# Kernel optimization log

Measured on AMD Instinct MI355X. Metric: run time of the kernel, lower is better.

## Reference

```python
import jax, jax.numpy as jnp
import numpy as np

B, A, D, K = 262144, 10, 10, 32  # batch, aspects, aspect dim (=10), projection dim


def setup_inputs() -> dict:
    key = jax.random.key(0)
    ks = jax.random.split(key, 7)
    scale = 0.01
    return {
        "user_rep": jax.random.normal(ks[0], (B, A, D), jnp.float32),
        "item_rep": jax.random.normal(ks[1], (B, A, D), jnp.float32),
        "affinity_matrix": jax.random.uniform(ks[2], (D, D), jnp.float32, -scale, scale),
        "user_projection": jax.random.uniform(ks[3], (K, D), jnp.float32, -scale, scale),
        "user_parameters": jax.random.uniform(ks[4], (K, 1), jnp.float32, -scale, scale),
        "item_projection": jax.random.uniform(ks[5], (K, D), jnp.float32, -scale, scale),
        "item_parameters": jax.random.uniform(ks[6], (K, 1), jnp.float32, -scale, scale),
    }


def reference(user_rep, item_rep, affinity_matrix, user_projection,
              user_parameters, item_projection, item_parameters):
    # affinity: relu( U @ M @ V^T )  -> [B, Au, Av]
    aff = jax.nn.relu(jnp.einsum('bud,de,bve->buv', user_rep, affinity_matrix, item_rep))

    h_user = jnp.einsum('kd,bud->bku', user_projection, user_rep)  # [B,K,Au]
    h_item = jnp.einsum('kd,bvd->bkv', item_projection, item_rep)  # [B,K,Av]

    # user importance branch
    hu = jax.nn.relu(h_user + jnp.einsum('bkv,buv->bku', h_item, aff))
    u_score = jnp.einsum('k,bku->bu', user_parameters[:, 0], hu)   # [B,Au]
    user_asp_importance = jax.nn.softmax(u_score, axis=1)

    # item importance branch
    hi = jax.nn.relu(h_item + jnp.einsum('bku,buv->bkv', h_user, aff))
    i_score = jnp.einsum('k,bkv->bv', item_parameters[:, 0], hi)   # [B,Av]
    item_asp_importance = jax.nn.softmax(i_score, axis=1)

    return (user_asp_importance, item_asp_importance)
```

## Files before the change

kernel.cpp:

```cpp
#include <hip/hip_runtime.h>
#include <hip/hip_bf16.h>

#define NB 262144
#define AA 10
#define DD 10
#define KK 32

static __device__ __forceinline__ float b2f(unsigned short h) {
    union { unsigned u; float f; } c; c.u = ((unsigned)h) << 16; return c.f;
}
static __device__ __forceinline__ float bflo(unsigned w) {
    union { unsigned u; float f; } c; c.u = w << 16; return c.f;
}
static __device__ __forceinline__ float bfhi(unsigned w) {
    union { unsigned u; float f; } c; c.u = w & 0xffff0000u; return c.f;
}

__device__ __forceinline__ int detect_f32(const unsigned short* p, int nshorts,
                                          unsigned expthr, int lane) {
    int bad = 0;
    if (lane < nshorts) {
        unsigned e = (p[lane] >> 7) & 0xFFu;
        bad = (e >= expthr);
    }
    return __any(bad);
}

__global__ __launch_bounds__(64, 1) void aie_kernel(
    const unsigned short* __restrict__ user_rep,
    const unsigned short* __restrict__ item_rep,
    const unsigned short* __restrict__ wM,
    const unsigned short* __restrict__ wPu,
    const unsigned short* __restrict__ wpu,
    const unsigned short* __restrict__ wPi,
    const unsigned short* __restrict__ wpi,
    float* __restrict__ out)
{
    __shared__ float sM[100];
    __shared__ float sPu[KK * DD], sPi[KK * DD], spu[KK], spi[KK];
    __shared__ float buf[6400];

    const int t = threadIdx.x;

    int f = 0;
    f |= detect_f32(user_rep, 64, 137, t) << 0;
    f |= detect_f32(item_rep, 64, 137, t) << 1;
    f |= detect_f32(wM,  64, 125, t) << 2;
    f |= detect_f32(wPu, 64, 125, t) << 3;
    f |= detect_f32(wpu, 32, 125, t) << 4;
    f |= detect_f32(wPi, 64, 125, t) << 5;
    f |= detect_f32(wpi, 32, 125, t) << 6;

    {
        const float* fM  = (const float*)wM;
        const float* fPu = (const float*)wPu;
        const float* fPi = (const float*)wPi;
        const float* fpu = (const float*)wpu;
        const float* fpi = (const float*)wpi;
        for (int i = t; i < 100; i += 64) sM[i] = (f & 4) ? fM[i] : b2f(wM[i]);
        for (int i = t; i < KK * DD; i += 64) {
            sPu[i] = (f & 8)  ? fPu[i] : b2f(wPu[i]);
            sPi[i] = (f & 32) ? fPi[i] : b2f(wPi[i]);
        }
        if (t < KK) {
            spu[t] = (f & 16) ? fpu[t] : b2f(wpu[t]);
            spi[t] = (f & 64) ? fpi[t] : b2f(wpi[t]);
        }
    }
    __syncthreads();

    const int blk = blockIdx.x;
    float U[AA][DD], V[AA][DD];

    if (f & 2) {
        const float4* g = (const float4*)((const float*)item_rep + (size_t)blk * 6400);
        #pragma unroll
        for (int j = 0; j < 25; j++) ((float4*)buf)[t + 64 * j] = g[t + 64 * j];
    } else {
        const uint2* g = (const uint2*)(item_rep + (size_t)blk * 6400);
        #pragma unroll
        for (int j = 0; j < 25; j++) {
            uint2 w = g[t + 64 * j];
            ((float4*)buf)[t + 64 * j] =
                make_float4(bflo(w.x), bfhi(w.x), bflo(w.y), bfhi(w.y));
        }
    }
    __syncthreads();
    {
        const float4* mine = (const float4*)(buf + 100 * t);
        #pragma unroll
        for (int j = 0; j < 25; j++) {
            float4 w = mine[j]; int e = 4 * j;
            V[e / 10][e % 10]             = w.x;
            V[(e + 1) / 10][(e + 1) % 10] = w.y;
            V[(e + 2) / 10][(e + 2) % 10] = w.z;
            V[(e + 3) / 10][(e + 3) % 10] = w.w;
        }
    }
    __syncthreads();

    if (f & 1) {
        const float4* g = (const float4*)((const float*)user_rep + (size_t)blk * 6400);
        #pragma unroll
        for (int j = 0; j < 25; j++) ((float4*)buf)[t + 64 * j] = g[t + 64 * j];
    } else {
        const uint2* g = (const uint2*)(user_rep + (size_t)blk * 6400);
        #pragma unroll
        for (int j = 0; j < 25; j++) {
            uint2 w = g[t + 64 * j];
            ((float4*)buf)[t + 64 * j] =
                make_float4(bflo(w.x), bfhi(w.x), bflo(w.y), bfhi(w.y));
        }
    }
    __syncthreads();
    {
        const float4* mine = (const float4*)(buf + 100 * t);
        #pragma unroll
        for (int j = 0; j < 25; j++) {
            float4 w = mine[j]; int e = 4 * j;
            U[e / 10][e % 10]             = w.x;
            U[(e + 1) / 10][(e + 1) % 10] = w.y;
            U[(e + 2) / 10][(e + 2) % 10] = w.z;
            U[(e + 3) / 10][(e + 3) % 10] = w.w;
        }
    }
    __syncthreads();

    float W[AA][DD];
    #pragma unroll
    for (int u = 0; u < AA; u++) {
        float um[DD];
        #pragma unroll
        for (int e = 0; e < DD; e++) {
            float a = U[u][0] * sM[e];
            #pragma unroll
            for (int d = 1; d < DD; d++) a += U[u][d] * sM[d * 10 + e];
            um[e] = a;
        }
        float wrow[DD];
        #pragma unroll
        for (int d = 0; d < DD; d++) wrow[d] = 0.f;
        #pragma unroll
        for (int v = 0; v < AA; v++) {
            float r = um[0] * V[v][0];
            #pragma unroll
            for (int e = 1; e < DD; e++) r += um[e] * V[v][e];
            r = fmaxf(r, 0.f);
            #pragma unroll
            for (int d = 0; d < DD; d++) wrow[d] += r * V[v][d];
        }
        #pragma unroll
        for (int d = 0; d < DD; d++) W[u][d] = wrow[d];
    }

    float us[AA];
    #pragma unroll
    for (int u = 0; u < AA; u++) us[u] = 0.f;
    #pragma unroll 2
    for (int k = 0; k < KK; k++) {
        float pu[DD], pi[DD];
        #pragma unroll
        for (int d = 0; d < DD; d++) { pu[d] = sPu[k * 10 + d]; pi[d] = sPi[k * 10 + d]; }
        const float wk = spu[k];
        #pragma unroll
        for (int u = 0; u < AA; u++) {
            float a = pu[0] * U[u][0], b = pi[0] * W[u][0];
            #pragma unroll
            for (int d = 1; d < DD; d++) { a += pu[d] * U[u][d]; b += pi[d] * W[u][d]; }
            us[u] += wk * fmaxf(a + b, 0.f);
        }
    }

    {
        float mx = us[0];
        #pragma unroll
        for (int u = 1; u < AA; u++) mx = fmaxf(mx, us[u]);
        float s = 0.f;
        #pragma unroll
        for (int u = 0; u < AA; u++) { us[u] = __expf(us[u] - mx); s += us[u]; }
        float inv = 1.f / s;
        #pragma unroll
        for (int u = 0; u < AA; u++) buf[11 * t + u] = us[u] * inv;
    }

    float X[AA][DD];
    #pragma unroll
    for (int u = 0; u < AA; u++) {
        float um[DD];
        #pragma unroll
        for (int e = 0; e < DD; e++) {
            float a = U[u][DD - 1] * sM[(DD - 1) * 10 + e];
            #pragma unroll
            for (int d = DD - 2; d >= 0; d--) a += U[u][d] * sM[d * 10 + e];
            um[e] = a;
        }
        #pragma unroll
        for (int v = 0; v < AA; v++) {
            float r = um[DD - 1] * V[v][DD - 1];
            #pragma unroll
            for (int e = DD - 2; e >= 0; e--) r += um[e] * V[v][e];
            r = fmaxf(r, 0.f);
            #pragma unroll
            for (int d = 0; d < DD; d++) {
                if (u == 0) X[v][d] = r * U[u][d];
                else        X[v][d] += r * U[u][d];
            }
        }
    }

    float isc[AA];
    #pragma unroll
    for (int v = 0; v < AA; v++) isc[v] = 0.f;
    #pragma unroll 2
    for (int k = 0; k < KK; k++) {
        float pu[DD], pi[DD];
        #pragma unroll
        for (int d = 0; d < DD; d++) { pu[d] = sPu[k * 10 + d]; pi[d] = sPi[k * 10 + d]; }
        const float wk = spi[k];
        #pragma unroll
        for (int v = 0; v < AA; v++) {
            float a = pi[0] * V[v][0], b = pu[0] * X[v][0];
            #pragma unroll
            for (int d = 1; d < DD; d++) { a += pi[d] * V[v][d]; b += pu[d] * X[v][d]; }
            isc[v] += wk * fmaxf(a + b, 0.f);
        }
    }

    {
        float mx = isc[0];
        #pragma unroll
        for (int v = 1; v < AA; v++) mx = fmaxf(mx, isc[v]);
        float s = 0.f;
        #pragma unroll
        for (int v = 0; v < AA; v++) { isc[v] = __expf(isc[v] - mx); s += isc[v]; }
        float inv = 1.f / s;
        #pragma unroll
        for (int v = 0; v < AA; v++) buf[704 + 11 * t + v] = isc[v] * inv;
    }
    __syncthreads();

    {
        float2* o0 = (float2*)(out + (size_t)blk * 640);
        float2* o1 = (float2*)(out + (size_t)NB * 10 + (size_t)blk * 640);
        #pragma unroll
        for (int j = 0; j < 5; j++) {
            int m = t + 64 * j;
            int i = m / 5;
            int u = 2 * (m - 5 * i);
            o0[m] = make_float2(buf[11 * i + u],       buf[11 * i + u + 1]);
            o1[m] = make_float2(buf[704 + 11 * i + u], buf[704 + 11 * i + u + 1]);
        }
    }
}

extern "C" void kernel_launch(void* const* d_in, const int* in_sizes, int n_in,
                              void* d_out, int out_size, void* d_ws, size_t ws_size,
                              hipStream_t stream) {
    const unsigned short* user_rep = (const unsigned short*)d_in[0];
    const unsigned short* item_rep = (const unsigned short*)d_in[1];
    const unsigned short* wM       = (const unsigned short*)d_in[2];
    const unsigned short* wPu      = (const unsigned short*)d_in[3];
    const unsigned short* wpu      = (const unsigned short*)d_in[4];
    const unsigned short* wPi      = (const unsigned short*)d_in[5];
    const unsigned short* wpi      = (const unsigned short*)d_in[6];
    float* out                     = (float*)d_out;

    dim3 block(64);
    dim3 grid(NB / 64);
    hipLaunchKernelGGL(aie_kernel, grid, block, 0, stream,
                       user_rep, item_rep, wM, wPu, wpu, wPi, wpi, out);
}
```

Before: 393.2 us.

## Split weight prep kernel, use packed float2 math, fuse K loop into per-aspect rows

Moves weight dtype detection and conversion into a separate one-block kernel that writes fp32 weights to workspace, which the main kernel reads as uniform global loads instead of staging them in shared memory. The main kernel loads each row's inputs directly per thread, with no shared-memory transpose or block barriers, and stores them as float2 vectors so the math can use packed FP32 ops. The K-projection loop is fused per aspect so the W/X intermediates no longer need full 10x10 register arrays, which lowers register pressure and lets launch bounds allow two waves. The costs are uncoalesced strided global loads per thread and an extra kernel launch.

```diff
diff --git a/kernel.cpp b/kernel.cpp
--- a/kernel.cpp
+++ b/kernel.cpp
@@ -1,11 +1,12 @@
 #include <hip/hip_runtime.h>
-#include <hip/hip_bf16.h>
 
 #define NB 262144
 #define AA 10
 #define DD 10
 #define KK 32
 
+typedef float v2f __attribute__((ext_vector_type(2)));
+
 static __device__ __forceinline__ float b2f(unsigned short h) {
     union { unsigned u; float f; } c; c.u = ((unsigned)h) << 16; return c.f;
 }
@@ -14,6 +15,9 @@
 }
 static __device__ __forceinline__ float bfhi(unsigned w) {
     union { unsigned u; float f; } c; c.u = w & 0xffff0000u; return c.f;
+}
+static __device__ __forceinline__ v2f mk2(float a, float b) {
+    v2f r; r.x = a; r.y = b; return r;
 }
 
 __device__ __forceinline__ int detect_f32(const unsigned short* p, int nshorts,
@@ -26,229 +30,213 @@
     return __any(bad);
 }
 
-__global__ __launch_bounds__(64, 1) void aie_kernel(
-    const unsigned short* __restrict__ user_rep,
-    const unsigned short* __restrict__ item_rep,
+__global__ __launch_bounds__(64) void prep_weights(
     const unsigned short* __restrict__ wM,
     const unsigned short* __restrict__ wPu,
     const unsigned short* __restrict__ wpu,
     const unsigned short* __restrict__ wPi,
     const unsigned short* __restrict__ wpi,
+    float* __restrict__ wf)
+{
+    const int t = threadIdx.x;
+    int f = 0;
+    f |= detect_f32(wM,  64, 125, t) << 0;
+    f |= detect_f32(wPu, 64, 125, t) << 1;
+    f |= detect_f32(wpu, 32, 125, t) << 2;
+    f |= detect_f32(wPi, 64, 125, t) << 3;
+    f |= detect_f32(wpi, 32, 125, t) << 4;
+    const float* fM  = (const float*)wM;
+    const float* fPu = (const float*)wPu;
+    const float* fpu = (const float*)wpu;
+    const float* fPi = (const float*)wPi;
+    const float* fpi = (const float*)wpi;
+    for (int i = t; i < 100; i += 64) wf[i]       = (f & 1)  ? fM[i]  : b2f(wM[i]);
+    for (int i = t; i < 320; i += 64) wf[100 + i] = (f & 2)  ? fPu[i] : b2f(wPu[i]);
+    if (t < 32)                       wf[420 + t] = (f & 4)  ? fpu[t] : b2f(wpu[t]);
+    for (int i = t; i < 320; i += 64) wf[452 + i] = (f & 8)  ? fPi[i] : b2f(wPi[i]);
+    if (t < 32)                       wf[772 + t] = (f & 16) ? fpi[t] : b2f(wpi[t]);
+}
+
+__global__ __launch_bounds__(64, 2) void aie_main(
+    const unsigned short* __restrict__ user_rep,
+    const unsigned short* __restrict__ item_rep,
+    const float* __restrict__ wf,
     float* __restrict__ out)
 {
-    __shared__ float sM[100];
-    __shared__ float sPu[KK * DD], sPi[KK * DD], spu[KK], spi[KK];
-    __shared__ float buf[6400];
-
+    __shared__ float obuf[1408];
     const int t = threadIdx.x;
-
-    int f = 0;
-    f |= detect_f32(user_rep, 64, 137, t) << 0;
-    f |= detect_f32(item_rep, 64, 137, t) << 1;
-    f |= detect_f32(wM,  64, 125, t) << 2;
-    f |= detect_f32(wPu, 64, 125, t) << 3;
-    f |= detect_f32(wpu, 32, 125, t) << 4;
-    f |= detect_f32(wPi, 64, 125, t) << 5;
-    f |= detect_f32(wpi, 32, 125, t) << 6;
-
-    {
-        const float* fM  = (const float*)wM;
-        const float* fPu = (const float*)wPu;
-        const float* fPi = (const float*)wPi;
-        const float* fpu = (const float*)wpu;
-        const float* fpi = (const float*)wpi;
-        for (int i = t; i < 100; i += 64) sM[i] = (f & 4) ? fM[i] : b2f(wM[i]);
-        for (int i = t; i < KK * DD; i += 64) {
-            sPu[i] = (f & 8)  ? fPu[i] : b2f(wPu[i]);
-            sPi[i] = (f & 32) ? fPi[i] : b2f(wPi[i]);
-        }
-        if (t < KK) {
-            spu[t] = (f & 16) ? fpu[t] : b2f(wpu[t]);
-            spi[t] = (f & 64) ? fpi[t] : b2f(wpi[t]);
-        }
-    }
-    __syncthreads();
-
-    const int blk = blockIdx.x;
-    float U[AA][DD], V[AA][DD];
-
-    if (f & 2) {
-        const float4* g = (const float4*)((const float*)item_rep + (size_t)blk * 6400);
-        #pragma unroll
-        for (int j = 0; j < 25; j++) ((float4*)buf)[t + 64 * j] = g[t + 64 * j];
+    const long long b = (long long)blockIdx.x * 64 + t;
+
+    const int fu = detect_f32(user_rep, 64, 137, t);
+    const int fi = detect_f32(item_rep, 64, 137, t);
+
+    v2f U2[AA][5], V2[AA][5];
+
+    if (fi) {
+        const float4* g = (const float4*)((const float*)item_rep + b * 100);
+        #pragma unroll
+        for (int j = 0; j < 25; j++) {
+            float4 w = g[j];
+            int p = 2 * j;
+            V2[p / 5][p % 5]             = mk2(w.x, w.y);
+            V2[(p + 1) / 5][(p + 1) % 5] = mk2(w.z, w.w);
+        }
     } else {
-        const uint2* g = (const uint2*)(item_rep + (size_t)blk * 6400);
-        #pragma unroll
-        for (int j = 0; j < 25; j++) {
-            uint2 w = g[t + 64 * j];
-            ((float4*)buf)[t + 64 * j] =
-                make_float4(bflo(w.x), bfhi(w.x), bflo(w.y), bfhi(w.y));
-        }
-    }
-    __syncthreads();
-    {
-        const float4* mine = (const float4*)(buf + 100 * t);
-        #pragma unroll
-        for (int j = 0; j < 25; j++) {
-            float4 w = mine[j]; int e = 4 * j;
-            V[e / 10][e % 10]             = w.x;
-            V[(e + 1) / 10][(e + 1) % 10] = w.y;
-            V[(e + 2) / 10][(e + 2) % 10] = w.z;
-            V[(e + 3) / 10][(e + 3) % 10] = w.w;
-        }
-    }
-    __syncthreads();
-
-    if (f & 1) {
-        const float4* g = (const float4*)((const float*)user_rep + (size_t)blk * 6400);
-        #pragma unroll
-        for (int j = 0; j < 25; j++) ((float4*)buf)[t + 64 * j] = g[t + 64 * j];
+        const uint2* g = (const uint2*)(item_rep + b * 100);
+        #pragma unroll
+        for (int j = 0; j < 25; j++) {
+            uint2 w = g[j];
+            int p = 2 * j;
+            V2[p / 5][p % 5]             = mk2(bflo(w.x), bfhi(w.x));
+            V2[(p + 1) / 5][(p + 1) % 5] = mk2(bflo(w.y), bfhi(w.y));
+        }
+    }
+    if (fu) {
+        const float4* g = (const float4*)((const float*)user_rep + b * 100);
+        #pragma unroll
+        for (int j = 0; j < 25; j++) {
+            float4 w = g[j];
+            int p = 2 * j;
+            U2[p / 5][p % 5]             = mk2(w.x, w.y);
+            U2[(p + 1) / 5][(p + 1) % 5] = mk2(w.z, w.w);
+        }
     } else {
-        const uint2* g = (const uint2*)(user_rep + (size_t)blk * 6400);
-        #pragma unroll
-        for (int j = 0; j < 25; j++) {
-            uint2 w = g[t + 64 * j];
-            ((float4*)buf)[t + 64 * j] =
-                make_float4(bflo(w.x), bfhi(w.x), bflo(w.y), bfhi(w.y));
-        }
-    }
-    __syncthreads();
-    {
-        const float4* mine = (const float4*)(buf + 100 * t);
-        #pragma unroll
-        for (int j = 0; j < 25; j++) {
-            float4 w = mine[j]; int e = 4 * j;
-            U[e / 10][e % 10]             = w.x;
-            U[(e + 1) / 10][(e + 1) % 10] = w.y;
-            U[(e + 2) / 10][(e + 2) % 10] = w.z;
-            U[(e + 3) / 10][(e + 3) % 10] = w.w;
-        }
-    }
-    __syncthreads();
-
-    float W[AA][DD];
+        const uint2* g = (const uint2*)(user_rep + b * 100);
+        #pragma unroll
+        for (int j = 0; j < 25; j++) {
+            uint2 w = g[j];
+            int p = 2 * j;
+            U2[p / 5][p % 5]             = mk2(bflo(w.x), bfhi(w.x));
+            U2[(p + 1) / 5][(p + 1) % 5] = mk2(bflo(w.y), bfhi(w.y));
+        }
+    }
+
+    const v2f*  M2  = (const v2f*)wf;
+    const v2f*  Pu2 = (const v2f*)(wf + 100);
+    const float* pu = wf + 420;
+    const v2f*  Pi2 = (const v2f*)(wf + 452);
+    const float* pi = wf + 772;
+
     #pragma unroll
     for (int u = 0; u < AA; u++) {
-        float um[DD];
-        #pragma unroll
-        for (int e = 0; e < DD; e++) {
-            float a = U[u][0] * sM[e];
-            #pragma unroll
-            for (int d = 1; d < DD; d++) a += U[u][d] * sM[d * 10 + e];
-            um[e] = a;
-        }
-        float wrow[DD];
-        #pragma unroll
-        for (int d = 0; d < DD; d++) wrow[d] = 0.f;
+        v2f um2[5];
+        {
+            const float x0 = U2[u][0].x;
+            #pragma unroll
+            for (int j = 0; j < 5; j++) um2[j] = x0 * M2[j];
+        }
+        #pragma unroll
+        for (int d = 1; d < DD; d++) {
+            const float x = (d & 1) ? U2[u][d >> 1].y : U2[u][d >> 1].x;
+            #pragma unroll
+            for (int j = 0; j < 5; j++) um2[j] += x * M2[d * 5 + j];
+        }
+        v2f Wr2[5];
+        #pragma unroll
+        for (int j = 0; j < 5; j++) Wr2[j] = mk2(0.f, 0.f);
         #pragma unroll
         for (int v = 0; v < AA; v++) {
-            float r = um[0] * V[v][0];
-            #pragma unroll
-            for (int e = 1; e < DD; e++) r += um[e] * V[v][e];
-            r = fmaxf(r, 0.f);
-            #pragma unroll
-            for (int d = 0; d < DD; d++) wrow[d] += r * V[v][d];
-        }
-        #pragma unroll
-        for (int d = 0; d < DD; d++) W[u][d] = wrow[d];
-    }
-
-    float us[AA];
+            v2f r2 = um2[0] * V2[v][0];
+            #pragma unroll
+            for (int j = 1; j < 5; j++) r2 += um2[j] * V2[v][j];
+            const float r = fmaxf(r2.x + r2.y, 0.f);
+            #pragma unroll
+            for (int j = 0; j < 5; j++) Wr2[j] += r * V2[v][j];
+        }
+        float acc = 0.f;
+        #pragma unroll 1
+        for (int k0 = 0; k0 < KK; k0 += 8) {
+            #pragma unroll
+            for (int kk = 0; kk < 8; kk++) {
+                const int k = k0 + kk;
+                v2f a2 = Pu2[k * 5] * U2[u][0];
+                v2f c2 = Pi2[k * 5] * Wr2[0];
+                #pragma unroll
+                for (int j = 1; j < 5; j++) {
+                    a2 += Pu2[k * 5 + j] * U2[u][j];
+                    c2 += Pi2[k * 5 + j] * Wr2[j];
+                }
+                const v2f s2 = a2 + c2;
+                acc += pu[k] * fmaxf(s2.x + s2.y, 0.f);
+            }
+        }
+        obuf[11 * t + u] = acc;
+    }
+
     #pragma unroll
-    for (int u = 0; u < AA; u++) us[u] = 0.f;
-    #pragma unroll 2
-    for (int k = 0; k < KK; k++) {
-        float pu[DD], pi[DD];
-        #pragma unroll
-        for (int d = 0; d < DD; d++) { pu[d] = sPu[k * 10 + d]; pi[d] = sPi[k * 10 + d]; }
-        const float wk = spu[k];
+    for (int v = 0; v < AA; v++) {
+        v2f mv2[5];
+        #pragma unroll
+        for (int dp = 0; dp < 5; dp++) {
+            v2f s0 = M2[(2 * dp) * 5]     * V2[v][0];
+            v2f s1 = M2[(2 * dp + 1) * 5] * V2[v][0];
+            #pragma unroll
+            for (int j = 1; j < 5; j++) {
+                s0 += M2[(2 * dp) * 5 + j]     * V2[v][j];
+                s1 += M2[(2 * dp + 1) * 5 + j] * V2[v][j];
+            }
+            mv2[dp] = mk2(s0.x + s0.y, s1.x + s1.y);
+        }
+        v2f Xr2[5];
+        #pragma unroll
+        for (int j = 0; j < 5; j++) Xr2[j] = mk2(0.f, 0.f);
         #pragma unroll
         for (int u = 0; u < AA; u++) {
-            float a = pu[0] * U[u][0], b = pi[0] * W[u][0];
-            #pragma unroll
-            for (int d = 1; d < DD; d++) { a += pu[d] * U[u][d]; b += pi[d] * W[u][d]; }
-            us[u] += wk * fmaxf(a + b, 0.f);
-        }
-    }
+            v2f r2 = mv2[0] * U2[u][0];
+            #pragma unroll
+            for (int j = 1; j < 5; j++) r2 += mv2[j] * U2[u][j];
+            const float r = fmaxf(r2.x + r2.y, 0.f);
+            #pragma unroll
+            for (int j = 0; j < 5; j++) Xr2[j] += r * U2[u][j];
+        }
+        float acc = 0.f;
+        #pragma unroll 1
+        for (int k0 = 0; k0 < KK; k0 += 8) {
+            #pragma unroll
+            for (int kk = 0; kk < 8; kk++) {
+                const int k = k0 + kk;
+                v2f a2 = Pi2[k * 5] * V2[v][0];
+                v2f c2 = Pu2[k * 5] * Xr2[0];
+                #pragma unroll
+                for (int j = 1; j < 5; j++) {
+                    a2 += Pi2[k * 5 + j] * V2[v][j];
+                    c2 += Pu2[k * 5 + j] * Xr2[j];
+                }
+                const v2f s2 = a2 + c2;
+                acc += pi[k] * fmaxf(s2.x + s2.y, 0.f);
+            }
+        }
+        obuf[704 + 11 * t + v] = acc;
+    }
+
+    #pragma unroll
+    for (int h = 0; h < 2; h++) {
+        const int base = 704 * h + 11 * t;
+        float s[AA];
+        #pragma unroll
+        for (int u = 0; u < AA; u++) s[u] = obuf[base + u];
+        float mx = s[0];
+        #pragma unroll
+        for (int u = 1; u < AA; u++) mx = fmaxf(mx, s[u]);
+        float sum = 0.f;
+        #pragma unroll
+        for (int u = 0; u < AA; u++) { s[u] = __expf(s[u] - mx); sum += s[u]; }
+        const float inv = 1.f / sum;
+        #pragma unroll
+        for (int u = 0; u < AA; u++) obuf[base + u] = s[u] * inv;
+    }
+    __syncthreads();
 
     {
-        float mx = us[0];
-        #pragma unroll
-        for (int u = 1; u < AA; u++) mx = fmaxf(mx, us[u]);
-        float s = 0.f;
-        #pragma unroll
-        for (int u = 0; u < AA; u++) { us[u] = __expf(us[u] - mx); s += us[u]; }
-        float inv = 1.f / s;
-        #pragma unroll
-        for (int u = 0; u < AA; u++) buf[11 * t + u] = us[u] * inv;
-    }
-
-    float X[AA][DD];
-    #pragma unroll
-    for (int u = 0; u < AA; u++) {
-        float um[DD];
-        #pragma unroll
-        for (int e = 0; e < DD; e++) {
-            float a = U[u][DD - 1] * sM[(DD - 1) * 10 + e];
-            #pragma unroll
-            for (int d = DD - 2; d >= 0; d--) a += U[u][d] * sM[d * 10 + e];
-            um[e] = a;
-        }
-        #pragma unroll
-        for (int v = 0; v < AA; v++) {
-            float r = um[DD - 1] * V[v][DD - 1];
-            #pragma unroll
-            for (int e = DD - 2; e >= 0; e--) r += um[e] * V[v][e];
-            r = fmaxf(r, 0.f);
-            #pragma unroll
-            for (int d = 0; d < DD; d++) {
-                if (u == 0) X[v][d] = r * U[u][d];
-                else        X[v][d] += r * U[u][d];
-            }
-        }
-    }
-
-    float isc[AA];
-    #pragma unroll
-    for (int v = 0; v < AA; v++) isc[v] = 0.f;
-    #pragma unroll 2
-    for (int k = 0; k < KK; k++) {
-        float pu[DD], pi[DD];
-        #pragma unroll
-        for (int d = 0; d < DD; d++) { pu[d] = sPu[k * 10 + d]; pi[d] = sPi[k * 10 + d]; }
-        const float wk = spi[k];
-        #pragma unroll
-        for (int v = 0; v < AA; v++) {
-            float a = pi[0] * V[v][0], b = pu[0] * X[v][0];
-            #pragma unroll
-            for (int d = 1; d < DD; d++) { a += pi[d] * V[v][d]; b += pu[d] * X[v][d]; }
-            isc[v] += wk * fmaxf(a + b, 0.f);
-        }
-    }
-
-    {
-        float mx = isc[0];
-        #pragma unroll
-        for (int v = 1; v < AA; v++) mx = fmaxf(mx, isc[v]);
-        float s = 0.f;
-        #pragma unroll
-        for (int v = 0; v < AA; v++) { isc[v] = __expf(isc[v] - mx); s += isc[v]; }
-        float inv = 1.f / s;
-        #pragma unroll
-        for (int v = 0; v < AA; v++) buf[704 + 11 * t + v] = isc[v] * inv;
-    }
-    __syncthreads();
-
-    {
-        float2* o0 = (float2*)(out + (size_t)blk * 640);
-        float2* o1 = (float2*)(out + (size_t)NB * 10 + (size_t)blk * 640);
+        float2* o0 = (float2*)(out + (size_t)blockIdx.x * 640);
+        float2* o1 = (float2*)(out + (size_t)NB * 10 + (size_t)blockIdx.x * 640);
         #pragma unroll
         for (int j = 0; j < 5; j++) {
             int m = t + 64 * j;
             int i = m / 5;
             int u = 2 * (m - 5 * i);
-            o0[m] = make_float2(buf[11 * i + u],       buf[11 * i + u + 1]);
-            o1[m] = make_float2(buf[704 + 11 * i + u], buf[704 + 11 * i + u + 1]);
+            o0[m] = make_float2(obuf[11 * i + u],       obuf[11 * i + u + 1]);
+            o1[m] = make_float2(obuf[704 + 11 * i + u], obuf[704 + 11 * i + u + 1]);
         }
     }
 }
@@ -258,15 +246,13 @@
                               hipStream_t stream) {
     const unsigned short* user_rep = (const unsigned short*)d_in[0];
     const unsigned short* item_rep = (const unsigned short*)d_in[1];
-    const unsigned short* wM       = (const unsigned short*)d_in[2];
-    const unsigned short* wPu      = (const unsigned short*)d_in[3];
-    const unsigned short* wpu      = (const unsigned short*)d_in[4];
-    const unsigned short* wPi      = (const unsigned short*)d_in[5];
-    const unsigned short* wpi      = (const unsigned short*)d_in[6];
-    float* out                     = (float*)d_out;
-
-    dim3 block(64);
-    dim3 grid(NB / 64);
-    hipLaunchKernelGGL(aie_kernel, grid, block, 0, stream,
-                       user_rep, item_rep, wM, wPu, wpu, wPi, wpi, out);
-}
+    float* wf = (float*)d_ws;
+
+    hipLaunchKernelGGL(prep_weights, dim3(1), dim3(64), 0, stream,
+                       (const unsigned short*)d_in[2], (const unsigned short*)d_in[3],
+                       (const unsigned short*)d_in[4], (const unsigned short*)d_in[5],
+                       (const unsigned short*)d_in[6], wf);
+
+    hipLaunchKernelGGL(aie_main, dim3(NB / 64), dim3(64), 0, stream,
+                       user_rep, item_rep, wf, (float*)d_out);
+}
```

After: 320.1 us. 1.23x faster.
